# Kernel optimization log

Measured on AMD Instinct MI355X. Metric: run time of the kernel, lower is better.

## Reference

```python
import math
import jax, jax.numpy as jnp
import numpy as np

B, S, DM, H, KH = 2, 2048, 1024, 16, 4
HD = DM // H          # 64
N_REP = H // KH       # 4
ROPE_THETA = 10000.0


def setup_inputs() -> dict:
    key = jax.random.key(0)
    ks = jax.random.split(key, 5)
    x = jax.random.normal(ks[0], (B, S, DM), dtype=jnp.float32)
    wq = jax.random.normal(ks[1], (H * HD, DM), dtype=jnp.float32) * 0.02
    wk = jax.random.normal(ks[2], (KH * HD, DM), dtype=jnp.float32) * 0.02
    wv = jax.random.normal(ks[3], (KH * HD, DM), dtype=jnp.float32) * 0.02
    wo = jax.random.normal(ks[4], (DM, H * HD), dtype=jnp.float32) * 0.02
    # freqs_cis = exp(i * t * theta^(-2j/d)) represented as cos/sin, shape [S, HD//2]
    inv_freq = 1.0 / (ROPE_THETA ** (jnp.arange(0, HD, 2, dtype=jnp.float32) / HD))
    angles = jnp.arange(S, dtype=jnp.float32)[:, None] * inv_freq[None, :]
    return {
        'x': x, 'wq': wq, 'wk': wk, 'wv': wv, 'wo': wo,
        'freqs_cos': jnp.cos(angles), 'freqs_sin': jnp.sin(angles),
    }


def _rope(t, cos, sin):
    # t: [B, S, h, HD]; pairs (even, odd) rotated as complex mul
    tr = t.reshape(*t.shape[:-1], HD // 2, 2)
    xr, xi = tr[..., 0], tr[..., 1]
    c = cos[None, :, None, :]  # [1, S, 1, HD//2]
    s = sin[None, :, None, :]
    out = jnp.stack([xr * c - xi * s, xr * s + xi * c], axis=-1)
    return out.reshape(t.shape)


def reference(x, wq, wk, wv, wo, freqs_cos, freqs_sin):
    b, s, _ = x.shape
    xq = (x @ wq.T).reshape(b, s, H, HD)
    xk = (x @ wk.T).reshape(b, s, KH, HD)
    xv = (x @ wv.T).reshape(b, s, KH, HD)
    xq = _rope(xq, freqs_cos, freqs_sin)
    xk = _rope(xk, freqs_cos, freqs_sin)
    # [B, h, S, HD]
    xq = xq.transpose(0, 2, 1, 3)
    xk = xk.transpose(0, 2, 1, 3)
    xv = xv.transpose(0, 2, 1, 3)
    # GQA: repeat_interleave kv heads to match query heads
    xk = jnp.repeat(xk, N_REP, axis=1)
    xv = jnp.repeat(xv, N_REP, axis=1)
    scale = 1.0 / math.sqrt(HD)
    scores = jnp.einsum('bhqd,bhkd->bhqk', xq, xk) * scale
    causal = jnp.tril(jnp.ones((s, s), dtype=bool))
    scores = jnp.where(causal[None, None], scores, jnp.finfo(scores.dtype).min)
    attn = jax.nn.softmax(scores, axis=-1)
    out = jnp.einsum('bhqk,bhkd->bhqd', attn, xv)
    out = out.transpose(0, 2, 1, 3).reshape(b, s, H * HD)
    return out @ wo.T
```

## Files before the change

kernel.cpp:

```cpp
#include <hip/hip_runtime.h>
#include <hip/hip_bf16.h>
#include <type_traits>

#define B_ 2
#define S_ 2048
#define DM_ 1024
#define H_ 16
#define KH_ 4
#define HD_ 64
#define NREP_ 4
#define QKV_LD 1536
#define CLOG 0.1803368801111244f
#define FIXM 8.0f

typedef float f32x4 __attribute__((ext_vector_type(4)));
typedef float f32x16 __attribute__((ext_vector_type(16)));
typedef short s16x8 __attribute__((ext_vector_type(8)));
typedef unsigned int u32x2 __attribute__((ext_vector_type(2)));

static __device__ __forceinline__ float bf2f(unsigned short u) {
  union { unsigned int u; float f; } x; x.u = ((unsigned int)u) << 16; return x.f;
}
static __device__ __forceinline__ unsigned short f2bf(float f) {
  union { float f; unsigned int u; } x; x.f = f;
  unsigned int r = (x.u + 0x7fffu + ((x.u >> 16) & 1u)) >> 16;
  return (unsigned short)r;
}
static __device__ __forceinline__ unsigned int cvtpk_bf16(float lo, float hi) {
  unsigned int r;
  asm("v_cvt_pk_bf16_f32 %0, %1, %2" : "=v"(r) : "v"(lo), "v"(hi));
  return r;
}
static __device__ __forceinline__ float fexp2(float x) {
  float r;
  asm("v_exp_f32 %0, %1" : "=v"(r) : "v"(x));
  return r;
}

__device__ __forceinline__ void gload_lds16(const unsigned short* g, unsigned short* l) {
  __builtin_amdgcn_global_load_lds(
      (const __attribute__((address_space(1))) unsigned int*)g,
      (__attribute__((address_space(3))) unsigned int*)l, 16, 0, 0);
}

__global__ void cvt_all_k(const float* __restrict__ x,
                          const float* __restrict__ wq, const float* __restrict__ wk,
                          const float* __restrict__ wv, const float* __restrict__ wo,
                          unsigned short* __restrict__ xb,
                          unsigned short* __restrict__ wqkv, unsigned short* __restrict__ wob) {
  int i = (blockIdx.x * 256 + threadIdx.x) * 4;
  const float* src; unsigned short* dst; int off;
  if (i < 4194304)      { src = x;  dst = xb;              off = i; }
  else if (i < 5242880) { src = wq; dst = wqkv;            off = i - 4194304; }
  else if (i < 5505024) { src = wk; dst = wqkv + 1048576;  off = i - 5242880; }
  else if (i < 5767168) { src = wv; dst = wqkv + 1310720;  off = i - 5505024; }
  else                  { src = wo; dst = wob;             off = i - 5767168; }
  float4 v = *(const float4*)(src + off);
  ushort4 o;
  o.x = f2bf(v.x); o.y = f2bf(v.y); o.z = f2bf(v.z); o.w = f2bf(v.w);
  *(ushort4*)(dst + off) = o;
}

#define BM 128
#define BN 128
#define BK 32

template <typename OT>
__global__ __launch_bounds__(512) void gemm_bt(const unsigned short* __restrict__ A,
                                               const unsigned short* __restrict__ Bw,
                                               OT* __restrict__ C,
                                               int M, int N, int K) {
  __shared__ unsigned short lds_a[BM * BK];
  __shared__ unsigned short lds_b[BN * BK];
  const int tid = threadIdx.x;
  const int wave = tid >> 6, lane = tid & 63;
  const int lr = lane & 15, lg = lane >> 4;
  const int m0 = blockIdx.y * BM, n0 = blockIdx.x * BN;
  const int wr = wave >> 2, wc = wave & 3;

  f32x4 acc[4][2] = {};

  const int srow = tid >> 2, scol = (tid & 3) << 3;

  for (int k0 = 0; k0 < K; k0 += BK) {
    gload_lds16(A + (size_t)(m0 + srow) * K + k0 + scol, &lds_a[tid * 8]);
    gload_lds16(Bw + (size_t)(n0 + srow) * K + k0 + scol, &lds_b[tid * 8]);
    __syncthreads();
    s16x8 af[4], bfr[2];
    #pragma unroll
    for (int mi = 0; mi < 4; ++mi)
      af[mi] = *(const s16x8*)&lds_a[(wr * 64 + mi * 16 + lr) * BK + lg * 8];
    #pragma unroll
    for (int ni = 0; ni < 2; ++ni)
      bfr[ni] = *(const s16x8*)&lds_b[(wc * 32 + ni * 16 + lr) * BK + lg * 8];
    #pragma unroll
    for (int mi = 0; mi < 4; ++mi) {
      #pragma unroll
      for (int ni = 0; ni < 2; ++ni)
        acc[mi][ni] = __builtin_amdgcn_mfma_f32_16x16x32_bf16(af[mi], bfr[ni], acc[mi][ni], 0, 0, 0);
    }
    __syncthreads();
  }
  #pragma unroll
  for (int mi = 0; mi < 4; ++mi) {
    #pragma unroll
    for (int ni = 0; ni < 2; ++ni) {
      #pragma unroll
      for (int r = 0; r < 4; ++r) {
        int row = m0 + wr * 64 + mi * 16 + lg * 4 + r;
        int col = n0 + wc * 32 + ni * 16 + lr;
        if constexpr (std::is_same<OT, unsigned short>::value)
          C[(size_t)row * N + col] = f2bf(acc[mi][ni][r]);
        else
          C[(size_t)row * N + col] = acc[mi][ni][r];
      }
    }
  }
}

__global__ void kvpack_k(const unsigned short* __restrict__ qkv,
                         const float* __restrict__ fc, const float* __restrict__ fs,
                         unsigned short* __restrict__ kp, unsigned short* __restrict__ vp) {
  int idx = blockIdx.x * 256 + threadIdx.x;
  int lane = idx & 63;
  int f  = (idx >> 6) & 3;
  int t  = (idx >> 8) & 63;
  int p  = idx >> 14;
  int b = p >> 2, kh = p & 3;
  int ql = lane & 31, hi = lane >> 5;
  {
    int s = t * 32 + ql;
    int d0 = f * 16 + hi * 8;
    const unsigned short* src = qkv + (size_t)(b * S_ + s) * QKV_LD + 1024 + kh * HD_ + d0;
    s16x8 v = *(const s16x8*)src;
    int i0 = d0 >> 1;
    float4 c4 = *(const float4*)(fc + s * 32 + i0);
    float4 s4 = *(const float4*)(fs + s * 32 + i0);
    float cc[4] = {c4.x, c4.y, c4.z, c4.w};
    float ss[4] = {s4.x, s4.y, s4.z, s4.w};
    union { s16x8 v; unsigned int w[4]; } o;
    #pragma unroll
    for (int e = 0; e < 4; ++e) {
      float xr = bf2f((unsigned short)v[2 * e]);
      float xi = bf2f((unsigned short)v[2 * e + 1]);
      o.w[e] = cvtpk_bf16(xr * cc[e] - xi * ss[e], xr * ss[e] + xi * cc[e]);
    }
    *(s16x8*)(kp + (size_t)idx * 8) = o.v;
  }
  {
    int d = (f >> 1) * 32 + ql;
    int kv0 = t * 32 + (f & 1) * 16 + hi * 8;
    const unsigned short* src = qkv + (size_t)(b * S_ + kv0) * QKV_LD + 1280 + kh * HD_ + d;
    s16x8 o;
    #pragma unroll
    for (int e = 0; e < 8; ++e) o[e] = (short)src[(size_t)e * QKV_LD];
    *(s16x8*)(vp + (size_t)idx * 8) = o;
  }
}

__global__ __launch_bounds__(256, 4) void attn_fwd13(const unsigned short* __restrict__ qkv,
                                                     const unsigned short* __restrict__ kp,
                                                     const unsigned short* __restrict__ vp,
                                                     const float* __restrict__ fc,
                                                     const float* __restrict__ fs,
                                                     unsigned short* __restrict__ ob) {
  __shared__ float mbuf[64][34];
  const int tid = threadIdx.x;
  const int wave = tid >> 6, lane = tid & 63;
  const int ql = lane & 31;
  const int hi = lane >> 5;
  const int bi = blockIdx.x;
  const int xcd = bi & 7;
  const int b = xcd >> 2, kh = xcd & 3;
  const int j = bi >> 3;
  const int h = kh * NREP_ + (j & 3);
  const int bt = j >> 2;

  int c, t0, t1;
  bool typeA = false, paired = false, doOut;
  if (bt < 32) {
    typeA = true; paired = true;
    c = 63 - bt;
    int T = c + 1;
    t0 = (wave * T) >> 2; t1 = ((wave + 1) * T) >> 2;
    doOut = (wave == 0);
  } else if (bt < 40) {
    paired = true;
    int bb2 = bt - 32;
    c = (wave < 2) ? (16 + bb2) : (31 - bb2);
    int T = c + 1, Th = T >> 1;
    if ((wave & 1) == 0) { t0 = 0;  t1 = Th; } else { t0 = Th; t1 = T; }
    doOut = (wave == 0) || (wave == 2);
  } else {
    c = (bt - 40) * 4 + wave;
    t0 = 0; t1 = c + 1;
    doOut = true;
  }
  const int q = c * 32 + ql;

  const unsigned short* qrow = qkv + (size_t)(b * S_ + q) * QKV_LD + h * HD_;
  s16x8 qf[4];
  #pragma unroll
  for (int ks = 0; ks < 4; ++ks) {
    s16x8 v = *(const s16x8*)(qrow + ks * 16 + hi * 8);
    int i0 = ks * 8 + hi * 4;
    float4 c4 = *(const float4*)(fc + q * 32 + i0);
    float4 s4 = *(const float4*)(fs + q * 32 + i0);
    float cc[4] = {c4.x, c4.y, c4.z, c4.w};
    float ss[4] = {s4.x, s4.y, s4.z, s4.w};
    union { s16x8 v; unsigned int w[4]; } o;
    #pragma unroll
    for (int e = 0; e < 4; ++e) {
      float xr = bf2f((unsigned short)v[2 * e]);
      float xi = bf2f((unsigned short)v[2 * e + 1]);
      o.w[e] = cvtpk_bf16(xr * cc[e] - xi * ss[e], xr * ss[e] + xi * cc[e]);
    }
    qf[ks] = o.v;
  }

  const unsigned short* kpt = kp + ((size_t)(b * KH_ + kh) << 17) + lane * 8;
  const unsigned short* vpt = vp + ((size_t)(b * KH_ + kh) << 17) + lane * 8;

  f32x16 oT0 = {};
  f32x16 oT1 = {};
  float l = 0.f;

  s16x8 ka[4], va[4];

#define LOADK(T) do { \
    const unsigned short* kp_ = kpt + ((size_t)(T) << 11); \
    ka[0] = *(const s16x8*)(kp_);        ka[1] = *(const s16x8*)(kp_ + 512); \
    ka[2] = *(const s16x8*)(kp_ + 1024); ka[3] = *(const s16x8*)(kp_ + 1536); \
  } while (0)
#define LOADV(T) do { \
    const unsigned short* vp_ = vpt + ((size_t)(T) << 11); \
    va[0] = *(const s16x8*)(vp_);        va[1] = *(const s16x8*)(vp_ + 512); \
    va[2] = *(const s16x8*)(vp_ + 1024); va[3] = *(const s16x8*)(vp_ + 1536); \
  } while (0)

  LOADK(t0);
  LOADV(t0);
  for (int t = t0; t < t1; ++t) {
    const bool diag = (t == c);
    const bool more = (t + 1 < t1);
    f32x16 st = {};
    __builtin_amdgcn_s_setprio(1);
    st = __builtin_amdgcn_mfma_f32_32x32x16_bf16(ka[0], qf[0], st, 0, 0, 0);
    st = __builtin_amdgcn_mfma_f32_32x32x16_bf16(ka[1], qf[1], st, 0, 0, 0);
    st = __builtin_amdgcn_mfma_f32_32x32x16_bf16(ka[2], qf[2], st, 0, 0, 0);
    st = __builtin_amdgcn_mfma_f32_32x32x16_bf16(ka[3], qf[3], st, 0, 0, 0);
    __builtin_amdgcn_s_setprio(0);
    if (more) LOADK(t + 1);
    if (diag) {
      #pragma unroll
      for (int r = 0; r < 16; ++r)
        if (((r & 3) + 8 * (r >> 2) + 4 * hi) > ql) st[r] = -1e30f;
    }
    #pragma unroll
    for (int ksv = 0; ksv < 2; ++ksv) {
      float pr[8];
      #pragma unroll
      for (int e = 0; e < 8; ++e)
        pr[e] = fexp2(fmaf(st[ksv * 8 + e], CLOG, -FIXM));
      l += ((pr[0] + pr[1]) + (pr[2] + pr[3])) + ((pr[4] + pr[5]) + (pr[6] + pr[7]));
      unsigned int a01 = cvtpk_bf16(pr[0], pr[1]);
      unsigned int a23 = cvtpk_bf16(pr[2], pr[3]);
      unsigned int b45 = cvtpk_bf16(pr[4], pr[5]);
      unsigned int b67 = cvtpk_bf16(pr[6], pr[7]);
      asm volatile("v_permlane32_swap_b32 %0, %1" : "+v"(a01), "+v"(b45));
      asm volatile("v_permlane32_swap_b32 %0, %1" : "+v"(a23), "+v"(b67));
      union { s16x8 v; unsigned int w[4]; } pb;
      pb.w[0] = a01; pb.w[1] = a23; pb.w[2] = b45; pb.w[3] = b67;
      __builtin_amdgcn_s_setprio(1);
      oT0 = __builtin_amdgcn_mfma_f32_32x32x16_bf16(va[ksv], pb.v, oT0, 0, 0, 0);
      oT1 = __builtin_amdgcn_mfma_f32_32x32x16_bf16(va[2 + ksv], pb.v, oT1, 0, 0, 0);
      __builtin_amdgcn_s_setprio(0);
    }
    if (more) LOADV(t + 1);
  }
#undef LOADK
#undef LOADV

#define WRITEP do { float* mp_ = &mbuf[lane][0]; \
    _Pragma("unroll") for (int r = 0; r < 16; ++r) { mp_[r] = oT0[r]; mp_[16 + r] = oT1[r]; } \
    mp_[32] = l; } while (0)
#define MERGEP do { float* mp_ = &mbuf[lane][0]; \
    l += mp_[32]; \
    _Pragma("unroll") for (int r = 0; r < 16; ++r) { \
      oT0[r] += mp_[r]; \
      oT1[r] += mp_[16 + r]; } } while (0)

  __syncthreads();
  if (paired && wave == 1) WRITEP;
  __syncthreads();
  if (paired && wave == 0) MERGEP;
  __syncthreads();
  if (paired && wave == 3) WRITEP;
  __syncthreads();
  if (paired && wave == 2) MERGEP;
  __syncthreads();
  if (typeA && wave == 2) WRITEP;
  __syncthreads();
  if (typeA && wave == 0) MERGEP;
#undef WRITEP
#undef MERGEP

  if (doOut) {
    float l_tot = l + __shfl_xor(l, 32);
    float invl = 1.0f / l_tot;
    unsigned short* orow = ob + (size_t)(b * S_ + q) * DM_ + h * HD_;
    #pragma unroll
    for (int dblk = 0; dblk < 2; ++dblk) {
      #pragma unroll
      for (int g = 0; g < 4; ++g) {
        float e0 = (dblk ? oT1[4 * g + 0] : oT0[4 * g + 0]) * invl;
        float e1 = (dblk ? oT1[4 * g + 1] : oT0[4 * g + 1]) * invl;
        float e2 = (dblk ? oT1[4 * g + 2] : oT0[4 * g + 2]) * invl;
        float e3 = (dblk ? oT1[4 * g + 3] : oT0[4 * g + 3]) * invl;
        u32x2 w;
        w.x = cvtpk_bf16(e0, e1);
        w.y = cvtpk_bf16(e2, e3);
        *(u32x2*)(orow + dblk * 32 + g * 8 + 4 * hi) = w;
      }
    }
  }
}

extern "C" void kernel_launch(void* const* d_in, const int* in_sizes, int n_in,
                              void* d_out, int out_size, void* d_ws, size_t ws_size,
                              hipStream_t stream) {
  const float* x  = (const float*)d_in[0];
  const float* wq = (const float*)d_in[1];
  const float* wk = (const float*)d_in[2];
  const float* wv = (const float*)d_in[3];
  const float* wo = (const float*)d_in[4];
  const float* fc = (const float*)d_in[5];
  const float* fs = (const float*)d_in[6];
  float* out = (float*)d_out;

  const size_t nX    = (size_t)B_ * S_ * DM_;
  const size_t nWQKV = (size_t)QKV_LD * DM_;
  const size_t nWO   = (size_t)DM_ * DM_;
  const size_t nQKV  = (size_t)B_ * S_ * QKV_LD;
  const size_t nKV   = (size_t)B_ * S_ * KH_ * HD_;

  unsigned short* xb    = (unsigned short*)d_ws;
  unsigned short* wqkv  = xb + nX;
  unsigned short* wob   = wqkv + nWQKV;
  unsigned short* qkv   = wob + nWO;
  unsigned short* kpk   = qkv + nQKV;
  unsigned short* vpk   = kpk + nKV;
  unsigned short* a_buf = vpk + nKV;

  const int M = B_ * S_;

  cvt_all_k<<<6656, 256, 0, stream>>>(x, wq, wk, wv, wo, xb, wqkv, wob);

  gemm_bt<unsigned short><<<dim3(QKV_LD / BN, M / BM), 512, 0, stream>>>(
      xb, wqkv, qkv, M, QKV_LD, DM_);

  kvpack_k<<<512, 256, 0, stream>>>(qkv, fc, fs, kpk, vpk);

  attn_fwd13<<<1408, 256, 0, stream>>>(qkv, kpk, vpk, fc, fs, a_buf);

  gemm_bt<float><<<dim3(DM_ / BN, M / BM), 512, 0, stream>>>(
      a_buf, wob, out, M, DM_, DM_);
}
```

Before: 99.52 us.

## Software-pipeline attention loop: overlap next tile's QK MFMA with current softmax

Restructures the attention inner loop into a two-stage software pipeline. K fragments are double-buffered (k0r/k1r), and the QK^T MFMAs for tile t+1 are issued between tile t's softmax and its PV MFMAs, so matrix-core work can overlap the exp/convert VALU work. The added register pressure is handled by lowering launch bounds from 4 to 3 waves per SIMD, which reduces occupancy.

```diff
diff --git a/kernel.cpp b/kernel.cpp
--- a/kernel.cpp
+++ b/kernel.cpp
@@ -158,7 +158,7 @@
   }
 }
 
-__global__ __launch_bounds__(256, 4) void attn_fwd13(const unsigned short* __restrict__ qkv,
+__global__ __launch_bounds__(256, 3) void attn_fwd14(const unsigned short* __restrict__ qkv,
                                                      const unsigned short* __restrict__ kp,
                                                      const unsigned short* __restrict__ vp,
                                                      const float* __restrict__ fc,
@@ -225,12 +225,12 @@
   f32x16 oT1 = {};
   float l = 0.f;
 
-  s16x8 ka[4], va[4];
-
-#define LOADK(T) do { \
+  s16x8 k0r[4], k1r[4], va[4];
+
+#define LOADKTO(T, KK) do { \
     const unsigned short* kp_ = kpt + ((size_t)(T) << 11); \
-    ka[0] = *(const s16x8*)(kp_);        ka[1] = *(const s16x8*)(kp_ + 512); \
-    ka[2] = *(const s16x8*)(kp_ + 1024); ka[3] = *(const s16x8*)(kp_ + 1536); \
+    KK[0] = *(const s16x8*)(kp_);        KK[1] = *(const s16x8*)(kp_ + 512); \
+    KK[2] = *(const s16x8*)(kp_ + 1024); KK[3] = *(const s16x8*)(kp_ + 1536); \
   } while (0)
 #define LOADV(T) do { \
     const unsigned short* vp_ = vpt + ((size_t)(T) << 11); \
@@ -238,19 +238,19 @@
     va[2] = *(const s16x8*)(vp_ + 1024); va[3] = *(const s16x8*)(vp_ + 1536); \
   } while (0)
 
-  LOADK(t0);
-  LOADV(t0);
-  for (int t = t0; t < t1; ++t) {
-    const bool diag = (t == c);
-    const bool more = (t + 1 < t1);
+  auto qk4 = [&](f32x16& dst, s16x8 (&KK)[4]) __attribute__((always_inline)) {
     f32x16 st = {};
     __builtin_amdgcn_s_setprio(1);
-    st = __builtin_amdgcn_mfma_f32_32x32x16_bf16(ka[0], qf[0], st, 0, 0, 0);
-    st = __builtin_amdgcn_mfma_f32_32x32x16_bf16(ka[1], qf[1], st, 0, 0, 0);
-    st = __builtin_amdgcn_mfma_f32_32x32x16_bf16(ka[2], qf[2], st, 0, 0, 0);
-    st = __builtin_amdgcn_mfma_f32_32x32x16_bf16(ka[3], qf[3], st, 0, 0, 0);
+    st = __builtin_amdgcn_mfma_f32_32x32x16_bf16(KK[0], qf[0], st, 0, 0, 0);
+    st = __builtin_amdgcn_mfma_f32_32x32x16_bf16(KK[1], qf[1], st, 0, 0, 0);
+    st = __builtin_amdgcn_mfma_f32_32x32x16_bf16(KK[2], qf[2], st, 0, 0, 0);
+    st = __builtin_amdgcn_mfma_f32_32x32x16_bf16(KK[3], qf[3], st, 0, 0, 0);
     __builtin_amdgcn_s_setprio(0);
-    if (more) LOADK(t + 1);
+    dst = st;
+  };
+
+  unsigned int pbw[8];
+  auto softmax = [&](f32x16& st, bool diag) __attribute__((always_inline)) {
     if (diag) {
       #pragma unroll
       for (int r = 0; r < 16; ++r)
@@ -269,16 +269,51 @@
       unsigned int b67 = cvtpk_bf16(pr[6], pr[7]);
       asm volatile("v_permlane32_swap_b32 %0, %1" : "+v"(a01), "+v"(b45));
       asm volatile("v_permlane32_swap_b32 %0, %1" : "+v"(a23), "+v"(b67));
+      pbw[ksv * 4 + 0] = a01; pbw[ksv * 4 + 1] = a23;
+      pbw[ksv * 4 + 2] = b45; pbw[ksv * 4 + 3] = b67;
+    }
+  };
+  auto pv = [&]() __attribute__((always_inline)) {
+    #pragma unroll
+    for (int ksv = 0; ksv < 2; ++ksv) {
       union { s16x8 v; unsigned int w[4]; } pb;
-      pb.w[0] = a01; pb.w[1] = a23; pb.w[2] = b45; pb.w[3] = b67;
+      pb.w[0] = pbw[ksv * 4 + 0]; pb.w[1] = pbw[ksv * 4 + 1];
+      pb.w[2] = pbw[ksv * 4 + 2]; pb.w[3] = pbw[ksv * 4 + 3];
       __builtin_amdgcn_s_setprio(1);
       oT0 = __builtin_amdgcn_mfma_f32_32x32x16_bf16(va[ksv], pb.v, oT0, 0, 0, 0);
       oT1 = __builtin_amdgcn_mfma_f32_32x32x16_bf16(va[2 + ksv], pb.v, oT1, 0, 0, 0);
       __builtin_amdgcn_s_setprio(0);
     }
-    if (more) LOADV(t + 1);
-  }
-#undef LOADK
+  };
+
+  f32x16 st0, st1;
+  LOADKTO(t0, k0r);
+  LOADV(t0);
+  qk4(st0, k0r);
+  int t = t0;
+  for (;;) {
+    {
+      bool more = t + 1 < t1;
+      if (more) LOADKTO(t + 1, k1r);
+      softmax(st0, t == c);
+      if (more) qk4(st1, k1r);
+      pv();
+      if (!more) break;
+      LOADV(t + 1);
+      ++t;
+    }
+    {
+      bool more = t + 1 < t1;
+      if (more) LOADKTO(t + 1, k0r);
+      softmax(st1, t == c);
+      if (more) qk4(st0, k0r);
+      pv();
+      if (!more) break;
+      LOADV(t + 1);
+      ++t;
+    }
+  }
+#undef LOADKTO
 #undef LOADV
 
 #define WRITEP do { float* mp_ = &mbuf[lane][0]; \
@@ -361,7 +396,7 @@
 
   kvpack_k<<<512, 256, 0, stream>>>(qkv, fc, fs, kpk, vpk);
 
-  attn_fwd13<<<1408, 256, 0, stream>>>(qkv, kpk, vpk, fc, fs, a_buf);
+  attn_fwd14<<<1408, 256, 0, stream>>>(qkv, kpk, vpk, fc, fs, a_buf);
 
   gemm_bt<float><<<dim3(DM_ / BN, M / BM), 512, 0, stream>>>(
       a_buf, wob, out, M, DM_, DM_);
```

Result: no change. 101.5 us (+2.0%).
